# Kernel optimization log

Hardware: AMD Instinct MI355X
Metric: run time of the kernel (lower is better)

Reference implementation:

```python
import jax, jax.numpy as jnp
import numpy as np

B, L, E, Q = 32, 2048, 512, 512

def setup_inputs() -> dict:
    key = jax.random.key(0)
    k1, k2, k3, k4, k5 = jax.random.split(key, 5)
    scale_attn = 1.0 / np.sqrt(E + Q)
    scale_v = 1.0 / np.sqrt(E)
    return {
        "embeddings": jax.random.normal(k1, (B, L, E), dtype=jnp.float32),
        "query": jax.random.normal(k2, (B, L, Q), dtype=jnp.float32),
        "W_attn": jax.random.normal(k3, (E, E + Q), dtype=jnp.float32) * scale_attn,
        "b_attn": jax.random.normal(k4, (E,), dtype=jnp.float32) * scale_attn,
        "v_w": jax.random.normal(k5, (E,), dtype=jnp.float32) * scale_v,
    }

def reference(embeddings, query, W_attn, b_attn, v_w):
    # concat along feature dim: (B, L, Q+E)
    cat = jnp.concatenate([query, embeddings], axis=2)
    # attn_layer: Linear(E+Q -> E), then tanh: (B, L, E)
    h = jnp.tanh(jnp.einsum('blf,ef->ble', cat, W_attn) + b_attn)
    # attn_v: Linear(E -> 1, no bias) -> scores (B, L)
    scores = jnp.einsum('ble,e->bl', h, v_w)
    # softmax over the sequence (dim=1 in torch)
    w = jax.nn.softmax(scores, axis=1)  # (B, L)
    # transpose to (B, 1, L) then bmm with embeddings -> (B, 1, E)
    applied = jnp.einsum('bl,ble->be', w, embeddings)[:, None, :]
    weights = w[:, None, :]
    return (applied, weights)
```

## Files before the change

kernel.cpp:

```cpp
#include <hip/hip_runtime.h>
#include <hip/hip_bf16.h>
#include <math.h>


typedef __attribute__((ext_vector_type(8))) short bf16x8;
typedef __attribute__((ext_vector_type(4))) float f32x4;

#define BDIM 32
#define LDIM 2048
#define EDIM 512
#define QDIM 512
#define KDIM 1024
#define MDIM (BDIM * LDIM)

#define BM 128
#define BN 128
#define BK 64
#define LDS_STRIDE (BK + 8)

__device__ inline unsigned int pack2bf(float lo, float hi) {
    unsigned int a = __builtin_bit_cast(unsigned int, lo) + 0x8000u;
    unsigned int b = __builtin_bit_cast(unsigned int, hi) + 0x8000u;
    return __builtin_amdgcn_perm(b, a, 0x07060302);
}

__global__ __launch_bounds__(256) void scores_kernel(
    const float* __restrict__ emb, const float* __restrict__ query,
    const float* __restrict__ W, const float* __restrict__ b_attn,
    const float* __restrict__ v_w, float* __restrict__ scores)
{
    __shared__ unsigned short As[BM][LDS_STRIDE];
    __shared__ unsigned short Bs[BN][LDS_STRIDE];

    const int tid = threadIdx.x;
    const int bid = blockIdx.x;
    const int xcd = bid & 7;
    const int slot = bid >> 3;
    const int mtile = xcd * 64 + (slot >> 2);
    const int ntile = slot & 3;
    const int m0 = mtile * BM;
    const int n0 = ntile * BN;

    const int lane = tid & 63;
    const int wv = tid >> 6;
    const int wm = (wv >> 1) * 64;
    const int wn = (wv & 1) * 64;
    const int quad = lane >> 4;
    const int ln = lane & 15;

    const int row16 = tid >> 4;
    const int col4  = (tid & 15) * 4;

    f32x4 acc[4][4];
    #pragma unroll
    for (int i = 0; i < 4; i++)
        #pragma unroll
        for (int j = 0; j < 4; j++)
            acc[i][j] = (f32x4){0.f, 0.f, 0.f, 0.f};

    for (int k0 = 0; k0 < KDIM; k0 += BK) {
        const float* asrc = (k0 < QDIM) ? query : emb;
        const int koff = (k0 < QDIM) ? k0 : (k0 - QDIM);
        #pragma unroll
        for (int p = 0; p < 8; p++) {
            const int r = p * 16 + row16;
            const float4 v = *(const float4*)(asrc + (size_t)(m0 + r) * 512 + koff + col4);
            uint2 pk;
            pk.x = pack2bf(v.x, v.y);
            pk.y = pack2bf(v.z, v.w);
            *(uint2*)&As[r][col4] = pk;
        }
        #pragma unroll
        for (int p = 0; p < 8; p++) {
            const int r = p * 16 + row16;
            const float4 v = *(const float4*)(W + (size_t)(n0 + r) * 1024 + k0 + col4);
            uint2 pk;
            pk.x = pack2bf(v.x, v.y);
            pk.y = pack2bf(v.z, v.w);
            *(uint2*)&Bs[r][col4] = pk;
        }
        __syncthreads();

        #pragma unroll
        for (int ks = 0; ks < 2; ks++) {
            bf16x8 af[4], bf[4];
            #pragma unroll
            for (int i = 0; i < 4; i++)
                af[i] = *(const bf16x8*)&As[wm + i * 16 + ln][ks * 32 + quad * 8];
            #pragma unroll
            for (int j = 0; j < 4; j++)
                bf[j] = *(const bf16x8*)&Bs[wn + j * 16 + ln][ks * 32 + quad * 8];
            #pragma unroll
            for (int i = 0; i < 4; i++)
                #pragma unroll
                for (int j = 0; j < 4; j++)
                    acc[i][j] = __builtin_amdgcn_mfma_f32_16x16x32_bf16(af[i], bf[j], acc[i][j], 0, 0, 0);
        }
        __syncthreads();
    }

    float bj[4], vj[4];
    #pragma unroll
    for (int j = 0; j < 4; j++) {
        const int n = n0 + wn + j * 16 + ln;
        bj[j] = b_attn[n];
        vj[j] = v_w[n];
    }
    #pragma unroll
    for (int i = 0; i < 4; i++) {
        #pragma unroll
        for (int r = 0; r < 4; r++) {
            float s = 0.f;
            #pragma unroll
            for (int j = 0; j < 4; j++)
                s += tanhf(acc[i][j][r] + bj[j]) * vj[j];
            #pragma unroll
            for (int off = 1; off < 16; off <<= 1)
                s += __shfl_xor(s, off, 64);
            if (ln == 0)
                atomicAdd(&scores[m0 + wm + i * 16 + quad * 4 + r], s);
        }
    }
}

__global__ __launch_bounds__(256) void softmax_apply_kernel(
    const float* __restrict__ emb, const float* __restrict__ scores,
    float* __restrict__ out_applied, float* __restrict__ out_weights)
{
    const int b = blockIdx.x >> 5;
    const int chunk = blockIdx.x & 31;
    const int l0 = chunk * 64;
    const int tid = threadIdx.x;
    const float* srow = scores + b * LDIM;

    __shared__ float red[4];
    __shared__ float wls[64];
    __shared__ float partial[128 * 4];

    float mx = -1e30f;
    #pragma unroll
    for (int t = 0; t < 8; t++) mx = fmaxf(mx, srow[tid + t * 256]);
    #pragma unroll
    for (int off = 1; off < 64; off <<= 1) mx = fmaxf(mx, __shfl_xor(mx, off, 64));
    if ((tid & 63) == 0) red[tid >> 6] = mx;
    __syncthreads();
    mx = fmaxf(fmaxf(red[0], red[1]), fmaxf(red[2], red[3]));

    float sm = 0.f;
    #pragma unroll
    for (int t = 0; t < 8; t++) sm += expf(srow[tid + t * 256] - mx);
    #pragma unroll
    for (int off = 1; off < 64; off <<= 1) sm += __shfl_xor(sm, off, 64);
    __syncthreads();
    if ((tid & 63) == 0) red[tid >> 6] = sm;
    __syncthreads();
    sm = red[0] + red[1] + red[2] + red[3];
    const float inv = 1.f / sm;

    if (tid < 64) {
        const float w = expf(srow[l0 + tid] - mx) * inv;
        wls[tid] = w;
        out_weights[(size_t)b * LDIM + l0 + tid] = w;
    }
    __syncthreads();

    const int half = tid >> 7;
    const int cg = tid & 127;
    float4 acc = {0.f, 0.f, 0.f, 0.f};
    const float* ebase = emb + ((size_t)b * LDIM + l0 + half) * EDIM + cg * 4;
    #pragma unroll 8
    for (int i = 0; i < 32; i++) {
        const float4 v = *(const float4*)(ebase + (size_t)2 * i * EDIM);
        const float w = wls[half + 2 * i];
        acc.x += w * v.x;
        acc.y += w * v.y;
        acc.z += w * v.z;
        acc.w += w * v.w;
    }
    if (half == 1) *(float4*)&partial[cg * 4] = acc;
    __syncthreads();
    if (half == 0) {
        const float4 p = *(const float4*)&partial[cg * 4];
        float* dst = out_applied + b * EDIM + cg * 4;
        atomicAdd(dst + 0, acc.x + p.x);
        atomicAdd(dst + 1, acc.y + p.y);
        atomicAdd(dst + 2, acc.z + p.z);
        atomicAdd(dst + 3, acc.w + p.w);
    }
}

extern "C" void kernel_launch(void* const* d_in, const int* in_sizes, int n_in,
                              void* d_out, int out_size, void* d_ws, size_t ws_size,
                              hipStream_t stream) {
    const float* emb    = (const float*)d_in[0];
    const float* query  = (const float*)d_in[1];
    const float* W      = (const float*)d_in[2];
    const float* b_attn = (const float*)d_in[3];
    const float* v_w    = (const float*)d_in[4];

    float* out     = (float*)d_out;
    float* applied = out;
    float* weights = out + BDIM * EDIM;
    float* scores  = (float*)d_ws;

    hipMemsetAsync(scores, 0, (size_t)MDIM * sizeof(float), stream);
    hipMemsetAsync(applied, 0, (size_t)BDIM * EDIM * sizeof(float), stream);

    scores_kernel<<<2048, 256, 0, stream>>>(emb, query, W, b_attn, v_w, scores);

    softmax_apply_kernel<<<1024, 256, 0, stream>>>(emb, scores, applied, weights);
}
```

Measured before the change: 407.8 us.

## Pre-convert W to swizzled bf16 and double-buffer GEMM with direct LDS loads

Adds a kernel that converts W to bf16 once per call into a workspace buffer, laid out with an XOR swizzle. The scores GEMM then streams B tiles into LDS with global_load_lds. The A tiles are register-prefetched and double-buffered in swizzled LDS, replacing the padded single-buffer layout, and compute is raised with s_setprio. This overlaps global loads with MFMA work and removes the repeated fp32-to-bf16 conversion of W in every tile. The softmax/apply kernel now uses smaller chunks and twice as many blocks, and loads scores once into registers. The costs are an extra kernel launch, more LDS per block, and more atomics.

```diff
diff --git a/kernel.cpp b/kernel.cpp
--- a/kernel.cpp
+++ b/kernel.cpp
@@ -16,21 +16,104 @@
 #define BM 128
 #define BN 128
 #define BK 64
-#define LDS_STRIDE (BK + 8)
-
-__device__ inline unsigned int pack2bf(float lo, float hi) {
+#define NSTEPS (KDIM / BK)
+
+__device__ __forceinline__ unsigned int pack2bf(float lo, float hi) {
     unsigned int a = __builtin_bit_cast(unsigned int, lo) + 0x8000u;
     unsigned int b = __builtin_bit_cast(unsigned int, hi) + 0x8000u;
     return __builtin_amdgcn_perm(b, a, 0x07060302);
 }
 
-__global__ __launch_bounds__(256) void scores_kernel(
+__global__ __launch_bounds__(256) void convert_w_kernel(
+    const float* __restrict__ W, unsigned short* __restrict__ Wsw)
+{
+    const int gid = blockIdx.x * 256 + threadIdx.x;
+    const int n  = gid >> 7;
+    const int jb = (gid & 127) * 16;
+    const int sb = jb ^ ((n & 7) << 4);
+    const float* src = W + (size_t)n * KDIM + (sb >> 2);
+    src = W + (size_t)n * KDIM + (sb >> 1);
+    const float4 a = *(const float4*)(src);
+    const float4 c = *(const float4*)(src + 4);
+    uint4 o;
+    o.x = pack2bf(a.x, a.y); o.y = pack2bf(a.z, a.w);
+    o.z = pack2bf(c.x, c.y); o.w = pack2bf(c.z, c.w);
+    *(uint4*)((char*)Wsw + (size_t)n * 2048 + jb) = o;
+}
+
+__device__ __forceinline__ bf16x8 lds_frag(const unsigned short* buf, int row, int cb) {
+    return *(const bf16x8*)((const char*)buf + row * 128 + (cb ^ ((row & 7) << 4)));
+}
+
+__device__ __forceinline__ void load_a(const float* __restrict__ emb,
+                                       const float* __restrict__ query,
+                                       int m0, int kstep, int arow, int acol,
+                                       float4 (&r)[8])
+{
+    const int k0 = kstep * BK;
+    const float* asrc = (k0 < QDIM) ? query : emb;
+    const int koff = (k0 < QDIM) ? k0 : (k0 - QDIM);
+    #pragma unroll
+    for (int p = 0; p < 8; p++)
+        r[p] = *(const float4*)(asrc + (size_t)(m0 + p * 16 + arow) * 512 + koff + acol);
+}
+
+__device__ __forceinline__ void write_a(unsigned short* buf, int arow, int acolb,
+                                        int axor, const float4 (&r)[8])
+{
+    #pragma unroll
+    for (int p = 0; p < 8; p++) {
+        uint2 pk;
+        pk.x = pack2bf(r[p].x, r[p].y);
+        pk.y = pack2bf(r[p].z, r[p].w);
+        *(uint2*)((char*)buf + (p * 16 + arow) * 128 + (acolb ^ axor)) = pk;
+    }
+}
+
+__device__ __forceinline__ void gll_b(const unsigned short* __restrict__ Wsw,
+                                      unsigned short* buf, int n0, int kstep,
+                                      int brow, int bcb, int wvoff)
+{
+    const size_t kb = (size_t)kstep * (BK * 2);
+    #pragma unroll
+    for (int p = 0; p < 4; p++) {
+        const char* g = (const char*)Wsw + (size_t)(n0 + p * 32 + brow) * 2048 + kb + bcb;
+        __builtin_amdgcn_global_load_lds(
+            (const __attribute__((address_space(1))) void*)g,
+            (__attribute__((address_space(3))) void*)((char*)buf + p * 4096 + wvoff),
+            16, 0, 0);
+    }
+}
+
+__device__ __forceinline__ void compute_step(const unsigned short* a_,
+                                             const unsigned short* b_,
+                                             int wm, int wn, int ln, int quad,
+                                             f32x4 (&acc)[4][4])
+{
+    __builtin_amdgcn_s_setprio(1);
+    #pragma unroll
+    for (int ks = 0; ks < 2; ks++) {
+        bf16x8 af[4], bf_[4];
+        #pragma unroll
+        for (int i = 0; i < 4; i++) af[i] = lds_frag(a_, wm + i * 16 + ln, ks * 64 + quad * 16);
+        #pragma unroll
+        for (int j = 0; j < 4; j++) bf_[j] = lds_frag(b_, wn + j * 16 + ln, ks * 64 + quad * 16);
+        #pragma unroll
+        for (int i = 0; i < 4; i++)
+            #pragma unroll
+            for (int j = 0; j < 4; j++)
+                acc[i][j] = __builtin_amdgcn_mfma_f32_16x16x32_bf16(af[i], bf_[j], acc[i][j], 0, 0, 0);
+    }
+    __builtin_amdgcn_s_setprio(0);
+}
+
+__global__ __launch_bounds__(256, 2) void scores_kernel(
     const float* __restrict__ emb, const float* __restrict__ query,
-    const float* __restrict__ W, const float* __restrict__ b_attn,
+    const unsigned short* __restrict__ Wsw, const float* __restrict__ b_attn,
     const float* __restrict__ v_w, float* __restrict__ scores)
 {
-    __shared__ unsigned short As[BM][LDS_STRIDE];
-    __shared__ unsigned short Bs[BN][LDS_STRIDE];
+    __shared__ __align__(16) unsigned short As[2][BM * BK];
+    __shared__ __align__(16) unsigned short Bs[2][BN * BK];
 
     const int tid = threadIdx.x;
     const int bid = blockIdx.x;
@@ -48,8 +131,14 @@
     const int quad = lane >> 4;
     const int ln = lane & 15;
 
-    const int row16 = tid >> 4;
-    const int col4  = (tid & 15) * 4;
+    const int arow  = tid >> 4;
+    const int acol  = (tid & 15) * 4;
+    const int acolb = acol * 2;
+    const int axor  = (arow & 7) << 4;
+
+    const int brow = tid >> 3;
+    const int bcb  = (tid & 7) * 16;
+    const int wvoff = __builtin_amdgcn_readfirstlane((tid >> 6) << 10);
 
     f32x4 acc[4][4];
     #pragma unroll
@@ -58,44 +147,27 @@
         for (int j = 0; j < 4; j++)
             acc[i][j] = (f32x4){0.f, 0.f, 0.f, 0.f};
 
-    for (int k0 = 0; k0 < KDIM; k0 += BK) {
-        const float* asrc = (k0 < QDIM) ? query : emb;
-        const int koff = (k0 < QDIM) ? k0 : (k0 - QDIM);
-        #pragma unroll
-        for (int p = 0; p < 8; p++) {
-            const int r = p * 16 + row16;
-            const float4 v = *(const float4*)(asrc + (size_t)(m0 + r) * 512 + koff + col4);
-            uint2 pk;
-            pk.x = pack2bf(v.x, v.y);
-            pk.y = pack2bf(v.z, v.w);
-            *(uint2*)&As[r][col4] = pk;
+    float4 ra[8], rb[8];
+
+    load_a(emb, query, m0, 0, arow, acol, ra);
+    write_a(&As[0][0], arow, acolb, axor, ra);
+    gll_b(Wsw, &Bs[0][0], n0, 0, brow, bcb, wvoff);
+    load_a(emb, query, m0, 1, arow, acol, rb);
+    __syncthreads();
+
+    for (int t = 0; t < NSTEPS; t += 2) {
+        if (t < NSTEPS - 2) load_a(emb, query, m0, t + 2, arow, acol, ra);
+        write_a(&As[1][0], arow, acolb, axor, rb);
+        gll_b(Wsw, &Bs[1][0], n0, t + 1, brow, bcb, wvoff);
+        compute_step(&As[0][0], &Bs[0][0], wm, wn, ln, quad, acc);
+        __syncthreads();
+
+        if (t + 1 < NSTEPS - 1) {
+            if (t + 1 < NSTEPS - 2) load_a(emb, query, m0, t + 3, arow, acol, rb);
+            write_a(&As[0][0], arow, acolb, axor, ra);
+            gll_b(Wsw, &Bs[0][0], n0, t + 2, brow, bcb, wvoff);
         }
-        #pragma unroll
-        for (int p = 0; p < 8; p++) {
-            const int r = p * 16 + row16;
-            const float4 v = *(const float4*)(W + (size_t)(n0 + r) * 1024 + k0 + col4);
-            uint2 pk;
-            pk.x = pack2bf(v.x, v.y);
-            pk.y = pack2bf(v.z, v.w);
-            *(uint2*)&Bs[r][col4] = pk;
-        }
-        __syncthreads();
-
-        #pragma unroll
-        for (int ks = 0; ks < 2; ks++) {
-            bf16x8 af[4], bf[4];
-            #pragma unroll
-            for (int i = 0; i < 4; i++)
-                af[i] = *(const bf16x8*)&As[wm + i * 16 + ln][ks * 32 + quad * 8];
-            #pragma unroll
-            for (int j = 0; j < 4; j++)
-                bf[j] = *(const bf16x8*)&Bs[wn + j * 16 + ln][ks * 32 + quad * 8];
-            #pragma unroll
-            for (int i = 0; i < 4; i++)
-                #pragma unroll
-                for (int j = 0; j < 4; j++)
-                    acc[i][j] = __builtin_amdgcn_mfma_f32_16x16x32_bf16(af[i], bf[j], acc[i][j], 0, 0, 0);
-        }
+        compute_step(&As[1][0], &Bs[1][0], wm, wn, ln, quad, acc);
         __syncthreads();
     }
 
@@ -127,19 +199,23 @@
     const float* __restrict__ emb, const float* __restrict__ scores,
     float* __restrict__ out_applied, float* __restrict__ out_weights)
 {
-    const int b = blockIdx.x >> 5;
-    const int chunk = blockIdx.x & 31;
-    const int l0 = chunk * 64;
+    const int b = blockIdx.x >> 6;
+    const int chunk = blockIdx.x & 63;
+    const int l0 = chunk * 32;
     const int tid = threadIdx.x;
-    const float* srow = scores + b * LDIM;
+    const float* srow = scores + (size_t)b * LDIM;
 
     __shared__ float red[4];
-    __shared__ float wls[64];
-    __shared__ float partial[128 * 4];
-
-    float mx = -1e30f;
-    #pragma unroll
-    for (int t = 0; t < 8; t++) mx = fmaxf(mx, srow[tid + t * 256]);
+    __shared__ float wls[32];
+    __shared__ float partial[512];
+
+    float sv[8];
+    #pragma unroll
+    for (int t = 0; t < 8; t++) sv[t] = srow[tid + t * 256];
+
+    float mx = sv[0];
+    #pragma unroll
+    for (int t = 1; t < 8; t++) mx = fmaxf(mx, sv[t]);
     #pragma unroll
     for (int off = 1; off < 64; off <<= 1) mx = fmaxf(mx, __shfl_xor(mx, off, 64));
     if ((tid & 63) == 0) red[tid >> 6] = mx;
@@ -148,7 +224,7 @@
 
     float sm = 0.f;
     #pragma unroll
-    for (int t = 0; t < 8; t++) sm += expf(srow[tid + t * 256] - mx);
+    for (int t = 0; t < 8; t++) sm += expf(sv[t] - mx);
     #pragma unroll
     for (int off = 1; off < 64; off <<= 1) sm += __shfl_xor(sm, off, 64);
     __syncthreads();
@@ -157,7 +233,7 @@
     sm = red[0] + red[1] + red[2] + red[3];
     const float inv = 1.f / sm;
 
-    if (tid < 64) {
+    if (tid < 32) {
         const float w = expf(srow[l0 + tid] - mx) * inv;
         wls[tid] = w;
         out_weights[(size_t)b * LDIM + l0 + tid] = w;
@@ -168,8 +244,8 @@
     const int cg = tid & 127;
     float4 acc = {0.f, 0.f, 0.f, 0.f};
     const float* ebase = emb + ((size_t)b * LDIM + l0 + half) * EDIM + cg * 4;
-    #pragma unroll 8
-    for (int i = 0; i < 32; i++) {
+    #pragma unroll
+    for (int i = 0; i < 16; i++) {
         const float4 v = *(const float4*)(ebase + (size_t)2 * i * EDIM);
         const float w = wls[half + 2 * i];
         acc.x += w * v.x;
@@ -181,7 +257,7 @@
     __syncthreads();
     if (half == 0) {
         const float4 p = *(const float4*)&partial[cg * 4];
-        float* dst = out_applied + b * EDIM + cg * 4;
+        float* dst = out_applied + (size_t)b * EDIM + cg * 4;
         atomicAdd(dst + 0, acc.x + p.x);
         atomicAdd(dst + 1, acc.y + p.y);
         atomicAdd(dst + 2, acc.z + p.z);
@@ -201,12 +277,16 @@
     float* out     = (float*)d_out;
     float* applied = out;
     float* weights = out + BDIM * EDIM;
+
     float* scores  = (float*)d_ws;
+    unsigned short* Wsw = (unsigned short*)((char*)d_ws + (size_t)MDIM * 4);
 
     hipMemsetAsync(scores, 0, (size_t)MDIM * sizeof(float), stream);
     hipMemsetAsync(applied, 0, (size_t)BDIM * EDIM * sizeof(float), stream);
 
-    scores_kernel<<<2048, 256, 0, stream>>>(emb, query, W, b_attn, v_w, scores);
-
-    softmax_apply_kernel<<<1024, 256, 0, stream>>>(emb, scores, applied, weights);
-}
+    convert_w_kernel<<<256, 256, 0, stream>>>(W, Wsw);
+
+    scores_kernel<<<2048, 256, 0, stream>>>(emb, query, Wsw, b_attn, v_w, scores);
+
+    softmax_apply_kernel<<<2048, 256, 0, stream>>>(emb, scores, applied, weights);
+}
```

Result: faster. 387.2 us (-5.1%).
